# Optimization experiments

Measured on AMD Instinct MI355X. Metric: run time of the kernel, lower is better.

The kernel has to match this reference:

```python
import jax, jax.numpy as jnp
import numpy as np

POOL_LEN = 256
EPS = 1e-5
WEIGHT_BITS = 2


def adaptive_avg_pool1d(x, out_len):
    """Faithful torch AdaptiveAvgPool1d: window i = [floor(i*L/out), ceil((i+1)*L/out)).
    Implemented via cumsum + static gathers (jit-friendly, vectorized)."""
    L = x.shape[-1]
    i = np.arange(out_len)
    starts = (i * L) // out_len
    ends = -((-(i + 1) * L) // out_len)  # integer ceil
    csum = jnp.cumsum(x, axis=-1)
    csum = jnp.concatenate([jnp.zeros(x.shape[:-1] + (1,), x.dtype), csum], axis=-1)
    counts = jnp.asarray(ends - starts, x.dtype)
    return (csum[..., ends] - csum[..., starts]) / counts


def quantize_weight(w, bits=WEIGHT_BITS):
    """2-bit symmetric uniform quantization, per-output-channel scale, STE."""
    qp = 2 ** (bits - 1) - 1          # +1
    qn = -(2 ** (bits - 1))           # -2
    scale = jnp.maximum(jnp.max(jnp.abs(w), axis=1, keepdims=True) / qp, 1e-8)
    w_q = jnp.clip(jnp.round(w / scale), qn, qp) * scale
    return w + jax.lax.stop_gradient(w_q - w)  # straight-through estimator


def setup_inputs() -> dict:
    key = jax.random.key(0)
    k1, k2, k3, kw = jax.random.split(key, 4)
    B = 64
    return {
        "stage1": jax.random.normal(k1, (B, 256, 5000), jnp.float32),
        "stage2": jax.random.normal(k2, (B, 128, 2500), jnp.float32),
        "stage3": jax.random.normal(k3, (B, 64, 625), jnp.float32),
        "alpha": jnp.ones((3,), jnp.float32) / 3.0,
        "weight": jax.random.normal(kw, (128, 448), jnp.float32) * 0.05,
        "bias": jnp.zeros((128,), jnp.float32),
        "gamma": jnp.ones((128,), jnp.float32),
        "beta": jnp.zeros((128,), jnp.float32),
    }


def reference(stage1, stage2, stage3, alpha, weight, bias, gamma, beta):
    w = jax.nn.softmax(alpha)
    s1 = adaptive_avg_pool1d(stage1, POOL_LEN) * w[0]
    s2 = adaptive_avg_pool1d(stage2, POOL_LEN) * w[1]
    s3 = adaptive_avg_pool1d(stage3, POOL_LEN) * w[2]
    fused = jnp.concatenate([s1, s2, s3], axis=1)  # (B, 448, 256)
    wq = quantize_weight(weight)
    y = jnp.einsum('oc,bcl->bol', wq, fused) + bias[None, :, None]  # (B, 128, 256)
    # BatchNorm1d (training mode: batch stats over N and L)
    mean = jnp.mean(y, axis=(0, 2))
    var = jnp.var(y, axis=(0, 2))
    yn = (y - mean[None, :, None]) * jax.lax.rsqrt(var + EPS)[None, :, None]
    yn = yn * gamma[None, :, None] + beta[None, :, None]
    act = jax.nn.elu(yn)
    return jnp.mean(act, axis=-1)  # (B, 128)
```

## Files before the change

kernel.cpp:

```cpp
#include <hip/hip_runtime.h>
#include <hip/hip_bf16.h>

#define EPSV 1e-5f

typedef __attribute__((ext_vector_type(8))) short short8v;
typedef __attribute__((ext_vector_type(4))) float float4v;

__device__ inline unsigned short f2bf(float x) {
  __hip_bfloat16 h = __float2bfloat16(x);
  return *reinterpret_cast<unsigned short*>(&h);
}
__device__ inline float bf2f(unsigned short b) {
  unsigned u = ((unsigned)b) << 16;
  float f;
  __builtin_memcpy(&f, &u, 4);
  return f;
}

template <int L, int MAXW>
__device__ __forceinline__ void pool_row_vec(
    const float* __restrict__ rowp, float wst,
    unsigned short* __restrict__ outp, float* __restrict__ row, int t) {
  constexpr int L4 = L / 4;
  constexpr int ITER = (L4 + 255) / 256;
  const float4v* rp4 = (const float4v*)rowp;
  #pragma unroll
  for (int i = 0; i < ITER; ++i) {
    int idx = t + 256 * i;
    if (ITER * 256 == L4 || idx < L4) {
      float4v v = __builtin_nontemporal_load(rp4 + idx);
      *(float4v*)&row[idx * 4] = v;
    }
  }
  if (t < MAXW) row[L + t] = 0.f;
  __syncthreads();
  int start = (t * L) >> 8;
  int end = ((t + 1) * L + 255) >> 8;
  int width = end - start;
  float s = 0.f;
  #pragma unroll
  for (int i = 0; i < MAXW; ++i) {
    float v = row[start + i];
    s += (i < width) ? v : 0.f;
  }
  outp[t] = f2bf(s / (float)width * wst);
}

template <int L, int MAXW>
__device__ __forceinline__ void pool_row_scalar(
    const float* __restrict__ rowp, float wst,
    unsigned short* __restrict__ outp, float* __restrict__ row, int t) {
  constexpr int ITER = (L + 255) / 256;
  #pragma unroll
  for (int i = 0; i < ITER; ++i) {
    int idx = t + 256 * i;
    if (idx < L) row[idx] = __builtin_nontemporal_load(rowp + idx);
  }
  if (t < MAXW) row[L + t] = 0.f;
  __syncthreads();
  int start = (t * L) >> 8;
  int end = ((t + 1) * L + 255) >> 8;
  int width = end - start;
  float s = 0.f;
  #pragma unroll
  for (int i = 0; i < MAXW; ++i) {
    float v = row[start + i];
    s += (i < width) ? v : 0.f;
  }
  outp[t] = f2bf(s / (float)width * wst);
}

__global__ __launch_bounds__(256) void pool_quant_kernel(
    const float* __restrict__ s1, const float* __restrict__ s2,
    const float* __restrict__ s3, const float* __restrict__ alpha,
    const float* __restrict__ w, unsigned short* __restrict__ fusedb,
    unsigned short* __restrict__ qbf, float* __restrict__ scales) {
  __shared__ float row[5024];
  int bid = blockIdx.x;
  int t = threadIdx.x;

  if (bid >= 28672) {
    int o = bid - 28672;
    const float* wr = w + o * 448;
    float m = 0.f;
    for (int c = t; c < 448; c += 256) m = fmaxf(m, fabsf(wr[c]));
    float* sm = row;
    for (int off = 32; off; off >>= 1) m = fmaxf(m, __shfl_down(m, off, 64));
    if ((t & 63) == 0) sm[t >> 6] = m;
    __syncthreads();
    m = fmaxf(fmaxf(sm[0], sm[1]), fmaxf(sm[2], sm[3]));
    float scale = fmaxf(m, 1e-8f);
    for (int c = t; c < 448; c += 256) {
      float q = rintf(wr[c] / scale);
      q = fminf(fmaxf(q, -2.f), 1.f);
      qbf[o * 448 + c] = f2bf(q);
    }
    if (t == 0) scales[o] = scale;
    return;
  }

  float a0 = alpha[0], a1 = alpha[1], a2 = alpha[2];
  float mx = fmaxf(a0, fmaxf(a1, a2));
  float e0 = expf(a0 - mx), e1 = expf(a1 - mx), e2 = expf(a2 - mx);
  float esum = e0 + e1 + e2;

  if (bid < 16384) {
    int b = bid >> 8, c = bid & 255;
    const float* rowp = s1 + ((size_t)b * 256 + c) * 5000;
    unsigned short* outp = fusedb + ((size_t)b * 448 + c) * 256;
    pool_row_vec<5000, 21>(rowp, e0 / esum, outp, row, t);
  } else if (bid < 24576) {
    int q = bid - 16384;
    int b = q >> 7, c = q & 127;
    const float* rowp = s2 + ((size_t)b * 128 + c) * 2500;
    unsigned short* outp = fusedb + ((size_t)b * 448 + 256 + c) * 256;
    pool_row_vec<2500, 11>(rowp, e1 / esum, outp, row, t);
  } else {
    int q = bid - 24576;
    int b = q >> 6, c = q & 63;
    const float* rowp = s3 + ((size_t)b * 64 + c) * 625;
    unsigned short* outp = fusedb + ((size_t)b * 448 + 384 + c) * 256;
    pool_row_scalar<625, 4>(rowp, e2 / esum, outp, row, t);
  }
}

__global__ __launch_bounds__(256) void mfma_gemm_kernel(
    const unsigned short* __restrict__ qbf, const float* __restrict__ scales,
    const unsigned short* __restrict__ fusedb, const float* __restrict__ bias,
    unsigned short* __restrict__ ybf, float* __restrict__ Psum,
    float* __restrict__ Pssq) {
  __shared__ __align__(16) unsigned short Asm[64][40];
  __shared__ __align__(16) unsigned short Bsm[32][66];
  int b = blockIdx.z;
  int o0 = blockIdx.y * 64;
  int l0 = blockIdx.x * 64;
  int tid = threadIdx.x;
  int wave = tid >> 6, lane = tid & 63;
  int wm = wave >> 1, wn = wave & 1;
  int lrow = lane & 15, lg = lane >> 4;
  const unsigned short* Fp = fusedb + (size_t)b * 448 * 256;
  float4v acc[2][2];
  #pragma unroll
  for (int i = 0; i < 2; ++i)
    #pragma unroll
    for (int j = 0; j < 2; ++j) acc[i][j] = (float4v){0.f, 0.f, 0.f, 0.f};
  for (int c0 = 0; c0 < 448; c0 += 32) {
    { int r = tid >> 2, k0 = (tid & 3) * 8;
      *(short8v*)&Asm[r][k0] = *(const short8v*)(qbf + (size_t)(o0 + r) * 448 + c0 + k0); }
    { int k = tid >> 3, n0 = (tid & 7) * 8;
      short8v v = *(const short8v*)(Fp + (size_t)(c0 + k) * 256 + l0 + n0);
      *(short8v*)&Bsm[k][n0] = v; }
    __syncthreads();
    short8v af[2];
    #pragma unroll
    for (int mf = 0; mf < 2; ++mf)
      af[mf] = *(const short8v*)&Asm[wm * 32 + mf * 16 + lrow][lg * 8];
    #pragma unroll
    for (int nf = 0; nf < 2; ++nf) {
      int n = wn * 32 + nf * 16 + lrow;
      short8v bf;
      #pragma unroll
      for (int j = 0; j < 8; ++j) bf[j] = (short)Bsm[lg * 8 + j][n];
      #pragma unroll
      for (int mf = 0; mf < 2; ++mf)
        acc[mf][nf] = __builtin_amdgcn_mfma_f32_16x16x32_bf16(af[mf], bf, acc[mf][nf], 0, 0, 0);
    }
    __syncthreads();
  }
  float sv[2][4], qv[2][4];
  #pragma unroll
  for (int mf = 0; mf < 2; ++mf) {
    #pragma unroll
    for (int reg = 0; reg < 4; ++reg) {
      int r = o0 + wm * 32 + mf * 16 + lg * 4 + reg;
      float sc = scales[r], bv = bias[r];
      float s = 0.f, q = 0.f;
      #pragma unroll
      for (int nf = 0; nf < 2; ++nf) {
        int col = l0 + wn * 32 + nf * 16 + lrow;
        float val = acc[mf][nf][reg] * sc + bv;
        ybf[((size_t)b * 128 + r) * 256 + col] = f2bf(val);
        s += val; q += val * val;
      }
      sv[mf][reg] = s; qv[mf][reg] = q;
    }
  }
  #pragma unroll
  for (int mf = 0; mf < 2; ++mf)
    #pragma unroll
    for (int reg = 0; reg < 4; ++reg)
      #pragma unroll
      for (int m = 1; m < 16; m <<= 1) {
        sv[mf][reg] += __shfl_xor(sv[mf][reg], m, 64);
        qv[mf][reg] += __shfl_xor(qv[mf][reg], m, 64);
      }
  if (lrow == 0) {
    int slot = b * 8 + blockIdx.x * 2 + wn;
    #pragma unroll
    for (int mf = 0; mf < 2; ++mf)
      #pragma unroll
      for (int reg = 0; reg < 4; ++reg) {
        int r = o0 + wm * 32 + mf * 16 + lg * 4 + reg;
        Psum[r * 512 + slot] = sv[mf][reg];
        Pssq[r * 512 + slot] = qv[mf][reg];
      }
  }
}

__global__ __launch_bounds__(256) void final_kernel(
    const unsigned short* __restrict__ ybf, const float* __restrict__ Psum,
    const float* __restrict__ Pssq, const float* __restrict__ gamma,
    const float* __restrict__ beta, float* __restrict__ out) {
  int w = threadIdx.x >> 6;
  int lane = threadIdx.x & 63;
  int bo = blockIdx.x * 4 + w;
  int o = bo & 127;

  float s = 0.f, q = 0.f;
  const float* Pp = Psum + o * 512 + lane * 8;
  const float* Qp = Pssq + o * 512 + lane * 8;
  #pragma unroll
  for (int i = 0; i < 8; ++i) { s += Pp[i]; q += Qp[i]; }
  #pragma unroll
  for (int m = 1; m < 64; m <<= 1) {
    s += __shfl_xor(s, m, 64);
    q += __shfl_xor(q, m, 64);
  }
  float mean = s * (1.f / 16384.f);
  float var = q * (1.f / 16384.f) - mean * mean;
  float rs = rsqrtf(var + EPSV);
  float a = rs * gamma[o];
  float bb = beta[o] - mean * a;

  ushort4 v = *(const ushort4*)(ybf + (size_t)bo * 256 + lane * 4);
  float acc = 0.f;
  #pragma unroll
  for (int j = 0; j < 4; ++j) {
    float e = bf2f((&v.x)[j]);
    float yn = e * a + bb;
    acc += yn > 0.f ? yn : expm1f(yn);
  }
  for (int m = 32; m; m >>= 1) acc += __shfl_down(acc, m, 64);
  if (lane == 0) out[bo] = acc * (1.f / 256.f);
}

extern "C" void kernel_launch(void* const* d_in, const int* in_sizes, int n_in,
                              void* d_out, int out_size, void* d_ws, size_t ws_size,
                              hipStream_t stream) {
  const float* s1     = (const float*)d_in[0];
  const float* s2     = (const float*)d_in[1];
  const float* s3     = (const float*)d_in[2];
  const float* alpha  = (const float*)d_in[3];
  const float* weight = (const float*)d_in[4];
  const float* bias   = (const float*)d_in[5];
  const float* gamma  = (const float*)d_in[6];
  const float* beta   = (const float*)d_in[7];
  float* out = (float*)d_out;

  char* ws = (char*)d_ws;
  unsigned short* fusedb = (unsigned short*)ws;
  unsigned short* qbf    = (unsigned short*)(ws + 14680064);
  float* scales          = (float*)(ws + 14794752);
  unsigned short* ybf    = (unsigned short*)(ws + 14795264);
  float* Psum            = (float*)(ws + 18989568);
  float* Pssq            = (float*)(ws + 19251712);

  pool_quant_kernel<<<28800, 256, 0, stream>>>(s1, s2, s3, alpha, weight,
                                               fusedb, qbf, scales);
  dim3 g(4, 2, 64);
  mfma_gemm_kernel<<<g, 256, 0, stream>>>(qbf, scales, fusedb, bias, ybf,
                                          Psum, Pssq);
  final_kernel<<<2048, 256, 0, stream>>>(ybf, Psum, Pssq, gamma, beta, out);
}
```

Measured before the change: 100.7 us.

## Process multiple rows per pooling block with register prefetch; pack GEMM B tile in pairs

The pooling kernel now handles several rows per block (4, 8 or 16 depending on stage). Each block prefetches the next row into registers while the current row is summed from LDS, so global loads overlap with the reduction and the block count drops from 28800 to 5504. The GEMM stores the B tile as packed 32-bit pairs along K, so each MFMA operand is built from four 32-bit LDS reads instead of eight 16-bit ones. The trade-offs are more register pressure and fewer blocks available to hide memory latency in the bandwidth-bound pooling stage.

```diff
diff --git a/kernel.cpp b/kernel.cpp
--- a/kernel.cpp
+++ b/kernel.cpp
@@ -4,6 +4,7 @@
 #define EPSV 1e-5f
 
 typedef __attribute__((ext_vector_type(8))) short short8v;
+typedef __attribute__((ext_vector_type(4))) short short4v;
 typedef __attribute__((ext_vector_type(4))) float float4v;
 
 __device__ inline unsigned short f2bf(float x) {
@@ -17,57 +18,103 @@
   return f;
 }
 
-template <int L, int MAXW>
-__device__ __forceinline__ void pool_row_vec(
-    const float* __restrict__ rowp, float wst,
-    unsigned short* __restrict__ outp, float* __restrict__ row, int t) {
+__device__ __forceinline__ void bar_lds() {
+  asm volatile("s_waitcnt lgkmcnt(0)\n\ts_barrier" ::: "memory");
+}
+
+template <int L, int MAXW, int ROWS, int CH, int CHOFF>
+__device__ __forceinline__ void pool_rows_vec(
+    const float* __restrict__ srcBase, int row0, float wst,
+    unsigned short* __restrict__ fusedb, float* __restrict__ row, int t) {
   constexpr int L4 = L / 4;
-  constexpr int ITER = (L4 + 255) / 256;
-  const float4v* rp4 = (const float4v*)rowp;
-  #pragma unroll
-  for (int i = 0; i < ITER; ++i) {
-    int idx = t + 256 * i;
-    if (ITER * 256 == L4 || idx < L4) {
-      float4v v = __builtin_nontemporal_load(rp4 + idx);
-      *(float4v*)&row[idx * 4] = v;
+  constexpr int NLD = (L4 + 255) / 256;
+  float4v buf[NLD];
+  {
+    const float4v* rp = (const float4v*)(srcBase + (size_t)row0 * L);
+    #pragma unroll
+    for (int i = 0; i < NLD; ++i) {
+      int idx = t + 256 * i;
+      if (NLD * 256 == L4 || idx < L4) buf[i] = __builtin_nontemporal_load(rp + idx);
     }
   }
   if (t < MAXW) row[L + t] = 0.f;
-  __syncthreads();
-  int start = (t * L) >> 8;
-  int end = ((t + 1) * L + 255) >> 8;
-  int width = end - start;
-  float s = 0.f;
-  #pragma unroll
-  for (int i = 0; i < MAXW; ++i) {
-    float v = row[start + i];
-    s += (i < width) ? v : 0.f;
-  }
-  outp[t] = f2bf(s / (float)width * wst);
-}
-
-template <int L, int MAXW>
-__device__ __forceinline__ void pool_row_scalar(
-    const float* __restrict__ rowp, float wst,
-    unsigned short* __restrict__ outp, float* __restrict__ row, int t) {
-  constexpr int ITER = (L + 255) / 256;
-  #pragma unroll
-  for (int i = 0; i < ITER; ++i) {
-    int idx = t + 256 * i;
-    if (idx < L) row[idx] = __builtin_nontemporal_load(rowp + idx);
+  #pragma unroll 1
+  for (int r = 0; r < ROWS; ++r) {
+    #pragma unroll
+    for (int i = 0; i < NLD; ++i) {
+      int idx = t + 256 * i;
+      if (NLD * 256 == L4 || idx < L4) *(float4v*)&row[idx * 4] = buf[i];
+    }
+    bar_lds();
+    if (r + 1 < ROWS) {
+      const float4v* rpn = (const float4v*)(srcBase + (size_t)(row0 + r + 1) * L);
+      #pragma unroll
+      for (int i = 0; i < NLD; ++i) {
+        int idx = t + 256 * i;
+        if (NLD * 256 == L4 || idx < L4) buf[i] = __builtin_nontemporal_load(rpn + idx);
+      }
+    }
+    int start = (t * L) >> 8;
+    int end = ((t + 1) * L + 255) >> 8;
+    int width = end - start;
+    float s = 0.f;
+    #pragma unroll
+    for (int i = 0; i < MAXW; ++i) {
+      float v = row[start + i];
+      s += (i < width) ? v : 0.f;
+    }
+    int rr = row0 + r;
+    int b = rr / CH, c = rr % CH;
+    fusedb[((size_t)b * 448 + CHOFF + c) * 256 + t] = f2bf(s / (float)width * wst);
+    bar_lds();
+  }
+}
+
+template <int L, int MAXW, int ROWS, int CH, int CHOFF>
+__device__ __forceinline__ void pool_rows_scalar(
+    const float* __restrict__ srcBase, int row0, float wst,
+    unsigned short* __restrict__ fusedb, float* __restrict__ row, int t) {
+  constexpr int NLD = (L + 255) / 256;
+  float buf[NLD];
+  {
+    const float* rp = srcBase + (size_t)row0 * L;
+    #pragma unroll
+    for (int i = 0; i < NLD; ++i) {
+      int idx = t + 256 * i;
+      if (idx < L) buf[i] = __builtin_nontemporal_load(rp + idx);
+    }
   }
   if (t < MAXW) row[L + t] = 0.f;
-  __syncthreads();
-  int start = (t * L) >> 8;
-  int end = ((t + 1) * L + 255) >> 8;
-  int width = end - start;
-  float s = 0.f;
-  #pragma unroll
-  for (int i = 0; i < MAXW; ++i) {
-    float v = row[start + i];
-    s += (i < width) ? v : 0.f;
-  }
-  outp[t] = f2bf(s / (float)width * wst);
+  #pragma unroll 1
+  for (int r = 0; r < ROWS; ++r) {
+    #pragma unroll
+    for (int i = 0; i < NLD; ++i) {
+      int idx = t + 256 * i;
+      if (idx < L) row[idx] = buf[i];
+    }
+    bar_lds();
+    if (r + 1 < ROWS) {
+      const float* rpn = srcBase + (size_t)(row0 + r + 1) * L;
+      #pragma unroll
+      for (int i = 0; i < NLD; ++i) {
+        int idx = t + 256 * i;
+        if (idx < L) buf[i] = __builtin_nontemporal_load(rpn + idx);
+      }
+    }
+    int start = (t * L) >> 8;
+    int end = ((t + 1) * L + 255) >> 8;
+    int width = end - start;
+    float s = 0.f;
+    #pragma unroll
+    for (int i = 0; i < MAXW; ++i) {
+      float v = row[start + i];
+      s += (i < width) ? v : 0.f;
+    }
+    int rr = row0 + r;
+    int b = rr / CH, c = rr % CH;
+    fusedb[((size_t)b * 448 + CHOFF + c) * 256 + t] = f2bf(s / (float)width * wst);
+    bar_lds();
+  }
 }
 
 __global__ __launch_bounds__(256) void pool_quant_kernel(
@@ -79,8 +126,8 @@
   int bid = blockIdx.x;
   int t = threadIdx.x;
 
-  if (bid >= 28672) {
-    int o = bid - 28672;
+  if (bid >= 5376) {
+    int o = bid - 5376;
     const float* wr = w + o * 448;
     float m = 0.f;
     for (int c = t; c < 448; c += 256) m = fmaxf(m, fabsf(wr[c]));
@@ -104,23 +151,12 @@
   float e0 = expf(a0 - mx), e1 = expf(a1 - mx), e2 = expf(a2 - mx);
   float esum = e0 + e1 + e2;
 
-  if (bid < 16384) {
-    int b = bid >> 8, c = bid & 255;
-    const float* rowp = s1 + ((size_t)b * 256 + c) * 5000;
-    unsigned short* outp = fusedb + ((size_t)b * 448 + c) * 256;
-    pool_row_vec<5000, 21>(rowp, e0 / esum, outp, row, t);
-  } else if (bid < 24576) {
-    int q = bid - 16384;
-    int b = q >> 7, c = q & 127;
-    const float* rowp = s2 + ((size_t)b * 128 + c) * 2500;
-    unsigned short* outp = fusedb + ((size_t)b * 448 + 256 + c) * 256;
-    pool_row_vec<2500, 11>(rowp, e1 / esum, outp, row, t);
+  if (bid < 4096) {
+    pool_rows_vec<5000, 21, 4, 256, 0>(s1, bid * 4, e0 / esum, fusedb, row, t);
+  } else if (bid < 5120) {
+    pool_rows_vec<2500, 11, 8, 128, 256>(s2, (bid - 4096) * 8, e1 / esum, fusedb, row, t);
   } else {
-    int q = bid - 24576;
-    int b = q >> 6, c = q & 63;
-    const float* rowp = s3 + ((size_t)b * 64 + c) * 625;
-    unsigned short* outp = fusedb + ((size_t)b * 448 + 384 + c) * 256;
-    pool_row_scalar<625, 4>(rowp, e2 / esum, outp, row, t);
+    pool_rows_scalar<625, 4, 16, 64, 384>(s3, (bid - 5120) * 16, e2 / esum, fusedb, row, t);
   }
 }
 
@@ -130,7 +166,7 @@
     unsigned short* __restrict__ ybf, float* __restrict__ Psum,
     float* __restrict__ Pssq) {
   __shared__ __align__(16) unsigned short Asm[64][40];
-  __shared__ __align__(16) unsigned short Bsm[32][66];
+  __shared__ __align__(16) unsigned Bsm32[16][66];
   int b = blockIdx.z;
   int o0 = blockIdx.y * 64;
   int l0 = blockIdx.x * 64;
@@ -147,9 +183,16 @@
   for (int c0 = 0; c0 < 448; c0 += 32) {
     { int r = tid >> 2, k0 = (tid & 3) * 8;
       *(short8v*)&Asm[r][k0] = *(const short8v*)(qbf + (size_t)(o0 + r) * 448 + c0 + k0); }
-    { int k = tid >> 3, n0 = (tid & 7) * 8;
-      short8v v = *(const short8v*)(Fp + (size_t)(c0 + k) * 256 + l0 + n0);
-      *(short8v*)&Bsm[k][n0] = v; }
+    {
+      int kp = tid >> 4, n0 = (tid & 15) * 4;
+      const unsigned short* g0 = Fp + (size_t)(c0 + 2 * kp) * 256 + l0 + n0;
+      short4v v0 = *(const short4v*)g0;
+      short4v v1 = *(const short4v*)(g0 + 256);
+      #pragma unroll
+      for (int j = 0; j < 4; ++j)
+        Bsm32[kp][n0 + j] =
+            (((unsigned)(unsigned short)v1[j]) << 16) | (unsigned short)v0[j];
+    }
     __syncthreads();
     short8v af[2];
     #pragma unroll
@@ -158,9 +201,11 @@
     #pragma unroll
     for (int nf = 0; nf < 2; ++nf) {
       int n = wn * 32 + nf * 16 + lrow;
+      int tmp[4];
+      #pragma unroll
+      for (int jj = 0; jj < 4; ++jj) tmp[jj] = (int)Bsm32[lg * 4 + jj][n];
       short8v bf;
-      #pragma unroll
-      for (int j = 0; j < 8; ++j) bf[j] = (short)Bsm[lg * 8 + j][n];
+      __builtin_memcpy(&bf, tmp, 16);
       #pragma unroll
       for (int mf = 0; mf < 2; ++mf)
         acc[mf][nf] = __builtin_amdgcn_mfma_f32_16x16x32_bf16(af[mf], bf, acc[mf][nf], 0, 0, 0);
@@ -265,8 +310,8 @@
   float* Psum            = (float*)(ws + 18989568);
   float* Pssq            = (float*)(ws + 19251712);
 
-  pool_quant_kernel<<<28800, 256, 0, stream>>>(s1, s2, s3, alpha, weight,
-                                               fusedb, qbf, scales);
+  pool_quant_kernel<<<5504, 256, 0, stream>>>(s1, s2, s3, alpha, weight,
+                                              fusedb, qbf, scales);
   dim3 g(4, 2, 64);
   mfma_gemm_kernel<<<g, 256, 0, stream>>>(qbf, scales, fusedb, bias, ybf,
                                           Psum, Pssq);
```

Measured after the change: 101.0 us. No clear change (+0.3%).
